# Kernel optimization log

Measured on AMD Instinct MI355X. Metric: run time of the kernel, lower is better.

The kernel has to match this reference:

```python
import jax, jax.numpy as jnp
from jax import lax
import numpy as np

B, N, C, NPOINT, K = 8, 4096, 64, 1024, 32
EPS = 1e-5
SLOPE = 0.1  # leakyrelu negative_slope


def setup_inputs() -> dict:
    key = jax.random.key(0)
    ks = jax.random.split(key, 8)
    d = {
        "xyz": jax.random.normal(ks[0], (B, N, 3), jnp.float32),
        "features": jax.random.normal(ks[1], (B, N, C), jnp.float32),
    }
    for i, n in enumerate(["w_t", "w1_0", "w2_0", "w1_1", "w2_1"]):
        d[n] = jax.random.normal(ks[2 + i], (C, C), jnp.float32) * 0.05
    for n in ["b_t", "b1_0", "b2_0", "b1_1", "b2_1"]:
        d[n] = jnp.zeros((C,), jnp.float32)
    for n in ["g_t", "g1_0", "g2_0", "g1_1", "g2_1"]:
        d[n] = jnp.ones((C,), jnp.float32)
    for n in ["beta_t", "beta1_0", "beta2_0", "beta1_1", "beta2_1"]:
        d[n] = jnp.zeros((C,), jnp.float32)
    return d


def leaky(x):
    return jnp.where(x >= 0, x, SLOPE * x)


def conv1(x, w, b):  # x: [M, Cin, K], w: [Cout, Cin] (1x1 conv)
    return jnp.einsum('mck,oc->mok', x, w) + b[None, :, None]


def bn(x, g, be):  # training-mode BatchNorm1d over (batch, spatial)
    mean = x.mean(axis=(0, 2), keepdims=True)
    var = x.var(axis=(0, 2), keepdims=True)
    return g[None, :, None] * (x - mean) / jnp.sqrt(var + EPS) + be[None, :, None]


def fps(xyz, npoint):
    """Farthest point sampling, deterministic start at index 0. -> [B, npoint] int32"""
    b, n, _ = xyz.shape
    def step(carry, _):
        dist, far = carry
        centroid = jnp.take_along_axis(xyz, far[:, None, None], axis=1)  # [B,1,3]
        d = jnp.sum((xyz - centroid) ** 2, -1)  # [B,N]
        dist = jnp.minimum(dist, d)
        return (dist, jnp.argmax(dist, -1)), far
    init = (jnp.full((b, n), 1e10, xyz.dtype), jnp.zeros((b,), jnp.int32))
    _, idxs = lax.scan(step, init, None, length=npoint)  # [npoint, B]
    return idxs.T


def sqdist(src, dst):  # [B,S,3],[B,N,3] -> [B,S,N]
    d = -2.0 * jnp.einsum('bsc,bnc->bsn', src, dst)
    d += jnp.sum(src ** 2, -1)[:, :, None]
    d += jnp.sum(dst ** 2, -1)[:, None, :]
    return d


def resblock(x, w1, b1, g1, be1, w2, b2, g2, be2):
    h = leaky(bn(conv1(x, w1, b1), g1, be1))
    h = bn(conv1(h, w2, b2), g2, be2)
    return leaky(h + x)


def reference(xyz, features, w_t, b_t, g_t, beta_t,
              w1_0, b1_0, g1_0, beta1_0, w2_0, b2_0, g2_0, beta2_0,
              w1_1, b1_1, g1_1, beta1_1, w2_1, b2_1, g2_1, beta2_1):
    fps_idx = fps(xyz, NPOINT)                                   # [B,S]
    new_xyz = jnp.take_along_axis(xyz, fps_idx[:, :, None], axis=1)  # [B,S,3]
    d = sqdist(new_xyz, xyz)                                     # [B,S,N]
    _, idx = lax.top_k(-d, K)                                    # k smallest -> [B,S,K]
    grouped = jax.vmap(lambda f, i: f[i])(features, idx)         # [B,S,K,C]
    x = grouped.transpose(0, 1, 3, 2).reshape(B * NPOINT, C, K)  # [B*S, C, K]
    x = leaky(bn(conv1(x, w_t, b_t), g_t, beta_t))
    x = resblock(x, w1_0, b1_0, g1_0, beta1_0, w2_0, b2_0, g2_0, beta2_0)
    x = resblock(x, w1_1, b1_1, g1_1, beta1_1, w2_1, b2_1, g2_1, beta2_1)
    nf = x.reshape(B, NPOINT, C, K).transpose(0, 2, 1, 3)        # [B,C,S,K]
    sub_features = nf.max(axis=-1)                               # [B,C,S]
    return (new_xyz.transpose(0, 2, 1), sub_features)
```

## Files before the change

### kernel.cpp

```cpp
#include <hip/hip_runtime.h>
#include <stdint.h>

#define NB 8
#define NN 4096
#define NC 64
#define NS 1024
#define NK 32
#define NQ (NB*NS)
#define NP (NQ*NK)
#define EPSBN 1e-5f

typedef unsigned long long u64;
typedef unsigned short u16;
typedef float v2f __attribute__((ext_vector_type(2)));
typedef short bf8_t __attribute__((ext_vector_type(8)));
typedef float f4_t __attribute__((ext_vector_type(4)));

__device__ __forceinline__ float lrelu(float x){ return x >= 0.0f ? x : 0.1f*x; }

__device__ __forceinline__ unsigned int fkey(float d){
    unsigned int fb = __float_as_uint(d);
    return (fb & 0x80000000u) ? ~fb : (fb | 0x80000000u);
}
__device__ __forceinline__ unsigned f2bf(float f){
    unsigned u = __float_as_uint(f);
    return (u + 0x7fffu + ((u >> 16) & 1u)) >> 16;
}
__device__ __forceinline__ float bflo(unsigned u){ return __uint_as_float(u << 16); }
__device__ __forceinline__ float bfhi(unsigned u){ return __uint_as_float(u & 0xffff0000u); }

__device__ __forceinline__ int wave_incl_add(int x){
    int v = x;
    {int o=__builtin_amdgcn_update_dpp(0,v,0x111,0xf,0xf,true); v+=o;}
    {int o=__builtin_amdgcn_update_dpp(0,v,0x112,0xf,0xf,true); v+=o;}
    {int o=__builtin_amdgcn_update_dpp(0,v,0x114,0xf,0xf,true); v+=o;}
    {int o=__builtin_amdgcn_update_dpp(0,v,0x118,0xf,0xf,true); v+=o;}
    {int o=__builtin_amdgcn_update_dpp(0,v,0x142,0xa,0xf,true); v+=o;}
    {int o=__builtin_amdgcn_update_dpp(0,v,0x143,0xc,0xf,true); v+=o;}
    return v;
}
__device__ __forceinline__ float row_sum16(float x){
    int v = __float_as_int(x);
    {int o=__builtin_amdgcn_update_dpp(0,v,0x111,0xf,0xf,true); v=__float_as_int(__int_as_float(v)+__int_as_float(o));}
    {int o=__builtin_amdgcn_update_dpp(0,v,0x112,0xf,0xf,true); v=__float_as_int(__int_as_float(v)+__int_as_float(o));}
    {int o=__builtin_amdgcn_update_dpp(0,v,0x114,0xf,0xf,true); v=__float_as_int(__int_as_float(v)+__int_as_float(o));}
    {int o=__builtin_amdgcn_update_dpp(0,v,0x118,0xf,0xf,true); v=__float_as_int(__int_as_float(v)+__int_as_float(o));}
    return __int_as_float(v);
}
__device__ __forceinline__ double wave_max_d(double x){
    int lo = __double2loint(x), hi = __double2hiint(x);
    #define FPS_STG(ctl) { \
        int nl=__builtin_amdgcn_update_dpp(lo,lo,ctl,0xf,0xf,false); \
        int nh=__builtin_amdgcn_update_dpp(hi,hi,ctl,0xf,0xf,false); \
        double mx=fmax(__hiloint2double(hi,lo), __hiloint2double(nh,nl)); \
        lo=__double2loint(mx); hi=__double2hiint(mx); }
    FPS_STG(0x111) FPS_STG(0x112) FPS_STG(0x114) FPS_STG(0x118) FPS_STG(0x142) FPS_STG(0x143)
    #undef FPS_STG
    int flo = __builtin_amdgcn_readlane(lo, 63);
    int fhi = __builtin_amdgcn_readlane(hi, 63);
    return __hiloint2double(fhi, flo);
}

__global__ __launch_bounds__(256,1) void fps_kernel(const float* __restrict__ xyz,
                                                    float* __restrict__ out0,
                                                    float* __restrict__ nxyz)
{
    __shared__ float4 sP[NN];
    __shared__ double slots[2][4];
    __shared__ int sFar[NS];
    const int b = blockIdx.x, t = threadIdx.x;
    const int lane = t & 63, wv = t >> 6;
    const float* base = xyz + (size_t)b*NN*3;
    for (int i = t; i < NN; i += 256){
        const float* pp = base + 3*i;
        sP[i] = (float4){pp[0], pp[1], pp[2], 0.0f};
    }
    __syncthreads();
    v2f PX[8], PY[8], PZ[8], D[8];
    int LO[16];
    const int pb = t*16;
    #pragma unroll
    for (int j = 0; j < 8; ++j){
        float4 p0 = sP[pb+2*j], p1 = sP[pb+2*j+1];
        PX[j] = (v2f){ p0.x, p1.x };
        PY[j] = (v2f){ p0.y, p1.y };
        PZ[j] = (v2f){ p0.z, p1.z };
        D[j]  = (v2f){ 1e10f, 1e10f };
    }
    #pragma unroll
    for (int j = 0; j < 16; ++j) LO[j] = (int)(~(unsigned)(pb + j));
    int far = 0;
    float cx = sP[0].x, cy = sP[0].y, cz = sP[0].z;
    for (int s = 0; s < NS; ++s){
        if (t == 255) sFar[s] = far;
        double best;
        {
            #pragma clang fp contract(off)
            v2f cx2 = (v2f){cx, cx}, cy2 = (v2f){cy, cy}, cz2 = (v2f){cz, cz};
            double b0 = -1.0, b1 = -1.0, b2 = -1.0, b3 = -1.0;
            #pragma unroll
            for (int j = 0; j < 8; ++j){
                v2f dx = PX[j] - cx2;
                v2f dy = PY[j] - cy2;
                v2f dz = PZ[j] - cz2;
                v2f dd = (dx*dx + dy*dy) + dz*dz;
                v2f nd = __builtin_elementwise_min(D[j], dd);
                D[j] = nd;
                double k0 = __hiloint2double(__float_as_int(nd.x), LO[2*j]);
                double k1 = __hiloint2double(__float_as_int(nd.y), LO[2*j+1]);
                if (j & 1){ b1 = fmax(b1, k0); b3 = fmax(b3, k1); }
                else      { b0 = fmax(b0, k0); b2 = fmax(b2, k1); }
            }
            best = fmax(fmax(b0, b1), fmax(b2, b3));
        }
        double wb = wave_max_d(best);
        const int par = s & 1;
        if (lane == 0) slots[par][wv] = wb;
        __syncthreads();
        double s0 = slots[par][0], s1 = slots[par][1];
        double s2 = slots[par][2], s3 = slots[par][3];
        double mm = fmax(fmax(s0, s1), fmax(s2, s3));
        far = (int)(~(unsigned)__double2loint(mm));
        float4 cc = sP[far];
        cx = cc.x; cy = cc.y; cz = cc.z;
    }
    __syncthreads();
    for (int s = t; s < NS; s += 256){
        const int f = sFar[s];
        float4 cc = sP[f];
        float* npq = nxyz + ((size_t)b*NS + s)*3;
        npq[0]=cc.x; npq[1]=cc.y; npq[2]=cc.z;
        out0[(b*3+0)*NS+s]=cc.x; out0[(b*3+1)*NS+s]=cc.y; out0[(b*3+2)*NS+s]=cc.z;
    }
}

__global__ __launch_bounds__(256,2) void knn_kernel(const float* __restrict__ xyz,
                                                    const float* __restrict__ nxyz,
                                                    int* __restrict__ kidx)
{
    const int t = threadIdx.x, lane = t & 63, w = t >> 6;
    const int q = blockIdx.x*4 + w;
    const int b = q >> 10;
    const float* base = xyz + (size_t)b*NN*3;
    const float* qp = nxyz + (size_t)q*3;
    const float qx = qp[0], qy = qp[1], qz = qp[2];
    const float qsq = __fadd_rn(__fadd_rn(__fmul_rn(qx,qx),__fmul_rn(qy,qy)),__fmul_rn(qz,qz));

    unsigned int key[64];
    #pragma unroll
    for (int i = 0; i < 64; ++i){
        const int idx = (i<<6) + lane;
        const float* pp = base + 3*idx;
        float x = pp[0], y = pp[1], z = pp[2];
        float dot = __fadd_rn(__fadd_rn(__fmul_rn(qx,x),__fmul_rn(qy,y)),__fmul_rn(qz,z));
        float psq = __fadd_rn(__fadd_rn(__fmul_rn(x,x),__fmul_rn(y,y)),__fmul_rn(z,z));
        float d = __fadd_rn(__fadd_rn(__fmul_rn(-2.0f,dot),qsq),psq);
        key[i] = fkey(d);
    }
    unsigned int pref = 0; int need = 32;
    for (int bit = 31; bit >= 0; --bit){
        const unsigned int bound = 1u << bit;
        int c = 0;
        #pragma unroll
        for (int i = 0; i < 64; ++i) c += ((key[i] ^ pref) < bound) ? 1 : 0;
        int tot = __builtin_amdgcn_readlane(wave_incl_add(c), 63);
        if (tot < need){ need -= tot; pref |= bound; }
    }
    const unsigned int T = pref;
    int cl = 0;
    #pragma unroll
    for (int i = 0; i < 64; ++i) cl += (key[i] < T) ? 1 : 0;
    int incl_cl = wave_incl_add(cl);
    int clx = incl_cl - cl;
    int tiebase = __builtin_amdgcn_readlane(incl_cl, 63);
    int* oq = kidx + (size_t)q*NK;
    int pos = clx;
    #pragma unroll
    for (int i = 0; i < 64; ++i){
        if (key[i] < T){ oq[pos] = (i<<6) + lane; ++pos; }
    }
    int tcount = 0;
    for (int i = 0; i < 64 && tcount < need; ++i){
        u64 m = __ballot(key[i] == T);
        int myrank = (int)__popcll(m & ((1ull << lane) - 1ull));
        if ((key[i] == T) && (tcount + myrank < need))
            oq[tiebase + tcount + myrank] = (i<<6) + lane;
        tcount += (int)__popcll(m);
    }
}

__global__ __launch_bounds__(256) void wtrans_kernel(const float* __restrict__ w0,
    const float* __restrict__ w1, const float* __restrict__ w2,
    const float* __restrict__ w3, const float* __restrict__ w4,
    u16* __restrict__ dst, float* __restrict__ sums)
{
    const float* s;
    switch (blockIdx.x){
        case 0: s = w0; break; case 1: s = w1; break; case 2: s = w2; break;
        case 3: s = w3; break; default: s = w4; break;
    }
    for (int i = threadIdx.x; i < 128; i += 256)
        sums[(size_t)blockIdx.x*128 + i] = 0.0f;
    u16* d = dst + (size_t)blockIdx.x*4096;
    for (int i = threadIdx.x; i < 4096; i += 256){
        const int f = i >> 9, lane = (i >> 3) & 63, j = i & 7;
        const int mt = f >> 1, h = f & 1;
        const int o = mt*16 + (lane & 15);
        const int c = h*32 + (lane >> 4)*8 + j;
        d[i] = (u16)f2bf(s[o*64 + c]);
    }
}

__device__ __forceinline__ void bn_affine_prologue(const float* __restrict__ sums,
    const float* __restrict__ g, const float* __restrict__ beta, float* sAff, int t)
{
    if (t < 64){
        float su = sums[t], sq = sums[64+t];
        float mean = su * (1.0f/(float)NP);
        float var  = fmaxf(sq * (1.0f/(float)NP) - mean*mean, 0.0f);
        float sc = g[t] * rsqrtf(var + EPSBN);
        sAff[t]    = sc;
        sAff[64+t] = beta[t] - mean*sc;
    }
}

template<int ACT>
__global__ __launch_bounds__(256,3) void conv_mfma_kernel(const u16* __restrict__ in,
    u16* __restrict__ out, const u16* __restrict__ wfrag, const float* __restrict__ bias,
    const float* __restrict__ sums, const float* __restrict__ g,
    const float* __restrict__ beta, float* __restrict__ pout)
{
    __shared__ float sStat[4*128];
    __shared__ float sAff[128];
    const int t = threadIdx.x, lane = t & 63, wv = t >> 6;
    const int n = lane & 15, q = lane >> 4;
    const int bb = blockIdx.x;

    float scr[16], shr[16];
    if (ACT){
        bn_affine_prologue(sums, g, beta, sAff, t);
        __syncthreads();
        #pragma unroll
        for (int h = 0; h < 2; ++h){
            float4 a0 = *(const float4*)(sAff + h*32 + q*8);
            float4 a1 = *(const float4*)(sAff + h*32 + q*8 + 4);
            float4 b0 = *(const float4*)(sAff + 64 + h*32 + q*8);
            float4 b1 = *(const float4*)(sAff + 64 + h*32 + q*8 + 4);
            scr[h*8+0]=a0.x; scr[h*8+1]=a0.y; scr[h*8+2]=a0.z; scr[h*8+3]=a0.w;
            scr[h*8+4]=a1.x; scr[h*8+5]=a1.y; scr[h*8+6]=a1.z; scr[h*8+7]=a1.w;
            shr[h*8+0]=b0.x; shr[h*8+1]=b0.y; shr[h*8+2]=b0.z; shr[h*8+3]=b0.w;
            shr[h*8+4]=b1.x; shr[h*8+5]=b1.y; shr[h*8+6]=b1.z; shr[h*8+7]=b1.w;
        }
    }
    bf8_t wf[8];
    #pragma unroll
    for (int f = 0; f < 8; ++f)
        wf[f] = *(const bf8_t*)(wfrag + (f*64 + lane)*8);
    f4_t bv[4];
    #pragma unroll
    for (int mt = 0; mt < 4; ++mt)
        bv[mt] = *(const f4_t*)(bias + mt*16 + q*4);

    float st1[16], st2[16];
    #pragma unroll
    for (int e = 0; e < 16; ++e){ st1[e] = 0.0f; st2[e] = 0.0f; }

    #pragma unroll
    for (int i = 0; i < 4; ++i){
        const int p0 = bb*256 + wv*64 + i*16;
        const u16* row = in + (size_t)(p0 + n)*64;
        bf8_t bf0, bf1;
        if (ACT){
            union { unsigned u[4]; bf8_t v; } B0, B1;
            uint4 r0 = *(const uint4*)(row + q*8);
            uint4 r1 = *(const uint4*)(row + 32 + q*8);
            const unsigned ra[4] = {r0.x, r0.y, r0.z, r0.w};
            const unsigned rb[4] = {r1.x, r1.y, r1.z, r1.w};
            #pragma unroll
            for (int d = 0; d < 4; ++d){
                float x0 = bflo(ra[d]), x1 = bfhi(ra[d]);
                float y0 = fmaf(scr[2*d],   x0, shr[2*d]);   y0 = lrelu(y0);
                float y1 = fmaf(scr[2*d+1], x1, shr[2*d+1]); y1 = lrelu(y1);
                B0.u[d] = f2bf(y0) | (f2bf(y1) << 16);
                float z0 = bflo(rb[d]), z1 = bfhi(rb[d]);
                float w0 = fmaf(scr[8+2*d],   z0, shr[8+2*d]);   w0 = lrelu(w0);
                float w1 = fmaf(scr[8+2*d+1], z1, shr[8+2*d+1]); w1 = lrelu(w1);
                B1.u[d] = f2bf(w0) | (f2bf(w1) << 16);
            }
            bf0 = B0.v; bf1 = B1.v;
        } else {
            bf0 = *(const bf8_t*)(row + q*8);
            bf1 = *(const bf8_t*)(row + 32 + q*8);
        }
        f4_t acc[4];
        #pragma unroll
        for (int mt = 0; mt < 4; ++mt){
            acc[mt] = (f4_t){0.f,0.f,0.f,0.f};
            acc[mt] = __builtin_amdgcn_mfma_f32_16x16x32_bf16(wf[mt*2+0], bf0, acc[mt], 0,0,0);
            acc[mt] = __builtin_amdgcn_mfma_f32_16x16x32_bf16(wf[mt*2+1], bf1, acc[mt], 0,0,0);
        }
        u16* orow = out + (size_t)(p0 + n)*64;
        #pragma unroll
        for (int mt = 0; mt < 4; ++mt){
            float v0 = acc[mt].x + bv[mt].x;
            float v1 = acc[mt].y + bv[mt].y;
            float v2 = acc[mt].z + bv[mt].z;
            float v3 = acc[mt].w + bv[mt].w;
            st1[mt*4+0] += v0; st2[mt*4+0] += v0*v0;
            st1[mt*4+1] += v1; st2[mt*4+1] += v1*v1;
            st1[mt*4+2] += v2; st2[mt*4+2] += v2*v2;
            st1[mt*4+3] += v3; st2[mt*4+3] += v3*v3;
            uint2 pk;
            pk.x = f2bf(v0) | (f2bf(v1) << 16);
            pk.y = f2bf(v2) | (f2bf(v3) << 16);
            *(uint2*)(orow + mt*16 + q*4) = pk;
        }
    }
    #pragma unroll
    for (int e = 0; e < 16; ++e){
        float r1 = row_sum16(st1[e]);
        float r2 = row_sum16(st2[e]);
        if (n == 15){
            const int ch = (e >> 2)*16 + q*4 + (e & 3);
            sStat[wv*128 + ch]      = r1;
            sStat[wv*128 + 64 + ch] = r2;
        }
    }
    __syncthreads();
    if (t < 128){
        float s = sStat[t] + sStat[128+t] + sStat[256+t] + sStat[384+t];
        atomicAdd(pout + t, s);
    }
}

__global__ __launch_bounds__(256,3) void gconv_mfma_kernel(const float* __restrict__ features,
    const int* __restrict__ kidx, u16* __restrict__ out,
    const u16* __restrict__ wfrag, const float* __restrict__ bias,
    float* __restrict__ pout)
{
    __shared__ float sStat[4*128];
    const int t = threadIdx.x, lane = t & 63, wv = t >> 6;
    const int n = lane & 15, q = lane >> 4;
    const int bb = blockIdx.x;

    bf8_t wf[8];
    #pragma unroll
    for (int f = 0; f < 8; ++f)
        wf[f] = *(const bf8_t*)(wfrag + (f*64 + lane)*8);
    f4_t bv[4];
    #pragma unroll
    for (int mt = 0; mt < 4; ++mt)
        bv[mt] = *(const f4_t*)(bias + mt*16 + q*4);

    float st1[16], st2[16];
    #pragma unroll
    for (int e = 0; e < 16; ++e){ st1[e] = 0.0f; st2[e] = 0.0f; }

    #pragma unroll
    for (int i = 0; i < 4; ++i){
        const int p0 = bb*256 + wv*64 + i*16;
        const int p = p0 + n;
        const int b = p >> 15;
        const int idx = kidx[p];
        const float* frow = features + ((size_t)b*NN + idx)*NC;
        union { unsigned u[4]; bf8_t v; } B0, B1;
        {
            float4 a0 = *(const float4*)(frow + q*8);
            float4 a1 = *(const float4*)(frow + q*8 + 4);
            B0.u[0] = f2bf(a0.x) | (f2bf(a0.y) << 16);
            B0.u[1] = f2bf(a0.z) | (f2bf(a0.w) << 16);
            B0.u[2] = f2bf(a1.x) | (f2bf(a1.y) << 16);
            B0.u[3] = f2bf(a1.z) | (f2bf(a1.w) << 16);
            float4 c0 = *(const float4*)(frow + 32 + q*8);
            float4 c1 = *(const float4*)(frow + 32 + q*8 + 4);
            B1.u[0] = f2bf(c0.x) | (f2bf(c0.y) << 16);
            B1.u[1] = f2bf(c0.z) | (f2bf(c0.w) << 16);
            B1.u[2] = f2bf(c1.x) | (f2bf(c1.y) << 16);
            B1.u[3] = f2bf(c1.z) | (f2bf(c1.w) << 16);
        }
        f4_t acc[4];
        #pragma unroll
        for (int mt = 0; mt < 4; ++mt){
            acc[mt] = (f4_t){0.f,0.f,0.f,0.f};
            acc[mt] = __builtin_amdgcn_mfma_f32_16x16x32_bf16(wf[mt*2+0], B0.v, acc[mt], 0,0,0);
            acc[mt] = __builtin_amdgcn_mfma_f32_16x16x32_bf16(wf[mt*2+1], B1.v, acc[mt], 0,0,0);
        }
        u16* orow = out + (size_t)p*64;
        #pragma unroll
        for (int mt = 0; mt < 4; ++mt){
            float v0 = acc[mt].x + bv[mt].x;
            float v1 = acc[mt].y + bv[mt].y;
            float v2 = acc[mt].z + bv[mt].z;
            float v3 = acc[mt].w + bv[mt].w;
            st1[mt*4+0] += v0; st2[mt*4+0] += v0*v0;
            st1[mt*4+1] += v1; st2[mt*4+1] += v1*v1;
            st1[mt*4+2] += v2; st2[mt*4+2] += v2*v2;
            st1[mt*4+3] += v3; st2[mt*4+3] += v3*v3;
            uint2 pk;
            pk.x = f2bf(v0) | (f2bf(v1) << 16);
            pk.y = f2bf(v2) | (f2bf(v3) << 16);
            *(uint2*)(orow + mt*16 + q*4) = pk;
        }
    }
    #pragma unroll
    for (int e = 0; e < 16; ++e){
        float r1 = row_sum16(st1[e]);
        float r2 = row_sum16(st2[e]);
        if (n == 15){
            const int ch = (e >> 2)*16 + q*4 + (e & 3);
            sStat[wv*128 + ch]      = r1;
            sStat[wv*128 + 64 + ch] = r2;
        }
    }
    __syncthreads();
    if (t < 128){
        float s = sStat[t] + sStat[128+t] + sStat[256+t] + sStat[384+t];
        atomicAdd(pout + t, s);
    }
}

__global__ __launch_bounds__(256,2) void resid_kernel(const u16* __restrict__ v,
    const u16* __restrict__ yt, u16* __restrict__ x2,
    const float* __restrict__ sumsV, const float* __restrict__ gV, const float* __restrict__ betaV,
    const float* __restrict__ sumsY, const float* __restrict__ gY, const float* __restrict__ betaY)
{
    __shared__ float sAV[128], sAY[128];
    const int t = threadIdx.x;
    bn_affine_prologue(sumsV, gV, betaV, sAV, t);
    if (t >= 64 && t < 128) bn_affine_prologue(sumsY, gY, betaY, sAY, t - 64);
    __syncthreads();
    const int dc = t & 31, rg = t >> 5;
    const int c0 = dc*2, c1 = c0 + 1;
    const float va0 = sAV[c0], vb0 = sAV[64+c0];
    const float va1 = sAV[c1], vb1 = sAV[64+c1];
    const float ya0 = sAY[c0], yb0 = sAY[64+c0];
    const float ya1 = sAY[c1], yb1 = sAY[64+c1];
    const unsigned* vp = (const unsigned*)v;
    const unsigned* yp = (const unsigned*)yt;
    unsigned* xp = (unsigned*)x2;
    const size_t base = (size_t)blockIdx.x*512;
    #pragma unroll 4
    for (int r = rg; r < 512; r += 8){
        const size_t e = (base + r)*32 + dc;
        unsigned uv = vp[e], uy = yp[e];
        float r0 = lrelu(fmaf(va0, bflo(uv), vb0) + lrelu(fmaf(ya0, bflo(uy), yb0)));
        float r1 = lrelu(fmaf(va1, bfhi(uv), vb1) + lrelu(fmaf(ya1, bfhi(uy), yb1)));
        xp[e] = f2bf(r0) | (f2bf(r1) << 16);
    }
}

__global__ __launch_bounds__(256,2) void final_kernel(const u16* __restrict__ v2,
    const u16* __restrict__ x2,
    const float* __restrict__ sums, const float* __restrict__ g, const float* __restrict__ beta,
    float* __restrict__ out1)
{
    __shared__ float sAff[128];
    const int t = threadIdx.x;
    bn_affine_prologue(sums, g, beta, sAff, t);
    __syncthreads();
    const int dc = t & 31, sg = t >> 5;
    const int c0 = dc*2, c1 = c0 + 1;
    const float a0 = sAff[c0], s0 = sAff[64+c0];
    const float a1 = sAff[c1], s1 = sAff[64+c1];
    const int s = blockIdx.x*8 + sg;
    const unsigned* vp = (const unsigned*)v2;
    const unsigned* xp = (const unsigned*)x2;
    float m0 = -3.0e38f, m1 = -3.0e38f;
    #pragma unroll 8
    for (int kk = 0; kk < 32; ++kk){
        const size_t e = ((size_t)s*32 + kk)*32 + dc;
        unsigned uv = vp[e], ux = xp[e];
        m0 = fmaxf(m0, lrelu(fmaf(a0, bflo(uv), s0) + bflo(ux)));
        m1 = fmaxf(m1, lrelu(fmaf(a1, bfhi(uv), s1) + bfhi(ux)));
    }
    const int b = s >> 10, sl = s & 1023;
    out1[((size_t)b*NC + c0)*NS + sl] = m0;
    out1[((size_t)b*NC + c1)*NS + sl] = m1;
}

extern "C" void kernel_launch(void* const* d_in, const int* in_sizes, int n_in,
                              void* d_out, int out_size, void* d_ws, size_t ws_size,
                              hipStream_t stream)
{
    const float* xyz      = (const float*)d_in[0];
    const float* features = (const float*)d_in[1];
    const float* w_t    = (const float*)d_in[2];
    const float* w1_0   = (const float*)d_in[3];
    const float* w2_0   = (const float*)d_in[4];
    const float* w1_1   = (const float*)d_in[5];
    const float* w2_1   = (const float*)d_in[6];
    const float* b_t    = (const float*)d_in[7];
    const float* b1_0   = (const float*)d_in[8];
    const float* b2_0   = (const float*)d_in[9];
    const float* b1_1   = (const float*)d_in[10];
    const float* b2_1   = (const float*)d_in[11];
    const float* g_t    = (const float*)d_in[12];
    const float* g1_0   = (const float*)d_in[13];
    const float* g2_0   = (const float*)d_in[14];
    const float* g1_1   = (const float*)d_in[15];
    const float* g2_1   = (const float*)d_in[16];
    const float* beta_t  = (const float*)d_in[17];
    const float* beta1_0 = (const float*)d_in[18];
    const float* beta2_0 = (const float*)d_in[19];
    const float* beta1_1 = (const float*)d_in[20];
    const float* beta2_1 = (const float*)d_in[21];

    float* out = (float*)d_out;

    float* nxyz = (float*)d_ws;
    int*   kidx = (int*)(nxyz + 24576);
    float* sums = (float*)(kidx + NP);
    u16*  bwt  = (u16*)(sums + 5*128);
    u16*  buf0 = bwt + 5*4096;
    u16*  buf1 = buf0 + (size_t)NP*NC;
    u16*  buf2 = buf1 + (size_t)NP*NC;

    float* sumsT  = sums + 0*128;
    float* sums10 = sums + 1*128;
    float* sums20 = sums + 2*128;
    float* sums11 = sums + 3*128;
    float* sums21 = sums + 4*128;

    wtrans_kernel<<<5, 256, 0, stream>>>(w_t, w1_0, w2_0, w1_1, w2_1, bwt, sums);
    fps_kernel<<<NB, 256, 0, stream>>>(xyz, out, nxyz);
    knn_kernel<<<NQ/4, 256, 0, stream>>>(xyz, nxyz, kidx);

    gconv_mfma_kernel<<<1024, 256, 0, stream>>>(features, kidx, buf1,
                                                bwt + 0*4096, b_t, sumsT);
    conv_mfma_kernel<1><<<1024, 256, 0, stream>>>(buf1, buf0, bwt + 1*4096, b1_0,
                                                  sumsT, g_t, beta_t, sums10);
    conv_mfma_kernel<1><<<1024, 256, 0, stream>>>(buf0, buf2, bwt + 2*4096, b2_0,
                                                  sums10, g1_0, beta1_0, sums20);
    resid_kernel<<<512, 256, 0, stream>>>(buf2, buf1, buf0,
                                          sums20, g2_0, beta2_0,
                                          sumsT, g_t, beta_t);
    conv_mfma_kernel<0><<<1024, 256, 0, stream>>>(buf0, buf1, bwt + 3*4096, b1_1,
                                                  nullptr, nullptr, nullptr, sums11);
    conv_mfma_kernel<1><<<1024, 256, 0, stream>>>(buf1, buf2, bwt + 4*4096, b2_1,
                                                  sums11, g1_1, beta1_1, sums21);
    final_kernel<<<1024, 256, 0, stream>>>(buf2, buf0,
                                           sums21, g2_1, beta2_1,
                                           out + (size_t)NB*3*NS);
}
```

Measured before the change: 1.010 ms.

## Overlap features bf16 conversion with FPS, spread BN stat atomics, SoA FPS points

Adds 512 extra blocks to the FPS launch that convert features to bf16 into a scratch buffer while the 8 FPS blocks run, so gconv reads pre-converted bf16 rows instead of converting floats per gather. BN statistic atomics are spread over 16 replica slots per channel to reduce atomic contention, and the prologue sums the replicas. FPS shared memory is switched from float4 AoS to separate X/Y/Z arrays, and its max reduction is collapsed into a single serial chain. Risks include FPS-block scheduling interference from the extra blocks and a longer dependency chain in the FPS inner loop.

```diff
diff --git a/kernel.cpp b/kernel.cpp
--- a/kernel.cpp
+++ b/kernel.cpp
@@ -9,6 +9,7 @@
 #define NQ (NB*NS)
 #define NP (NQ*NK)
 #define EPSBN 1e-5f
+#define NREP 16
 
 typedef unsigned long long u64;
 typedef unsigned short u16;
@@ -63,9 +64,24 @@
 
 __global__ __launch_bounds__(256,1) void fps_kernel(const float* __restrict__ xyz,
                                                     float* __restrict__ out0,
-                                                    float* __restrict__ nxyz)
-{
-    __shared__ float4 sP[NN];
+                                                    float* __restrict__ nxyz,
+                                                    const float* __restrict__ features,
+                                                    u16* __restrict__ fbf)
+{
+    if (blockIdx.x >= NB){
+        const int cb = blockIdx.x - NB;
+        const float4* src = (const float4*)features;
+        uint2* dst = (uint2*)fbf;
+        for (int i = cb*256 + threadIdx.x; i < NB*NN*NC/4; i += 512*256){
+            float4 v = src[i];
+            uint2 pk;
+            pk.x = f2bf(v.x) | (f2bf(v.y) << 16);
+            pk.y = f2bf(v.z) | (f2bf(v.w) << 16);
+            dst[i] = pk;
+        }
+        return;
+    }
+    __shared__ float sX[NN], sY[NN], sZ[NN];
     __shared__ double slots[2][4];
     __shared__ int sFar[NS];
     const int b = blockIdx.x, t = threadIdx.x;
@@ -73,7 +89,7 @@
     const float* base = xyz + (size_t)b*NN*3;
     for (int i = t; i < NN; i += 256){
         const float* pp = base + 3*i;
-        sP[i] = (float4){pp[0], pp[1], pp[2], 0.0f};
+        sX[i] = pp[0]; sY[i] = pp[1]; sZ[i] = pp[2];
     }
     __syncthreads();
     v2f PX[8], PY[8], PZ[8], D[8];
@@ -81,23 +97,22 @@
     const int pb = t*16;
     #pragma unroll
     for (int j = 0; j < 8; ++j){
-        float4 p0 = sP[pb+2*j], p1 = sP[pb+2*j+1];
-        PX[j] = (v2f){ p0.x, p1.x };
-        PY[j] = (v2f){ p0.y, p1.y };
-        PZ[j] = (v2f){ p0.z, p1.z };
+        PX[j] = (v2f){ sX[pb+2*j], sX[pb+2*j+1] };
+        PY[j] = (v2f){ sY[pb+2*j], sY[pb+2*j+1] };
+        PZ[j] = (v2f){ sZ[pb+2*j], sZ[pb+2*j+1] };
         D[j]  = (v2f){ 1e10f, 1e10f };
     }
     #pragma unroll
     for (int j = 0; j < 16; ++j) LO[j] = (int)(~(unsigned)(pb + j));
     int far = 0;
-    float cx = sP[0].x, cy = sP[0].y, cz = sP[0].z;
+    float cx = sX[0], cy = sY[0], cz = sZ[0];
     for (int s = 0; s < NS; ++s){
         if (t == 255) sFar[s] = far;
         double best;
         {
             #pragma clang fp contract(off)
             v2f cx2 = (v2f){cx, cx}, cy2 = (v2f){cy, cy}, cz2 = (v2f){cz, cz};
-            double b0 = -1.0, b1 = -1.0, b2 = -1.0, b3 = -1.0;
+            best = -1.0;
             #pragma unroll
             for (int j = 0; j < 8; ++j){
                 v2f dx = PX[j] - cx2;
@@ -106,12 +121,9 @@
                 v2f dd = (dx*dx + dy*dy) + dz*dz;
                 v2f nd = __builtin_elementwise_min(D[j], dd);
                 D[j] = nd;
-                double k0 = __hiloint2double(__float_as_int(nd.x), LO[2*j]);
-                double k1 = __hiloint2double(__float_as_int(nd.y), LO[2*j+1]);
-                if (j & 1){ b1 = fmax(b1, k0); b3 = fmax(b3, k1); }
-                else      { b0 = fmax(b0, k0); b2 = fmax(b2, k1); }
+                best = fmax(best, __hiloint2double(__float_as_int(nd.x), LO[2*j]));
+                best = fmax(best, __hiloint2double(__float_as_int(nd.y), LO[2*j+1]));
             }
-            best = fmax(fmax(b0, b1), fmax(b2, b3));
         }
         double wb = wave_max_d(best);
         const int par = s & 1;
@@ -121,16 +133,15 @@
         double s2 = slots[par][2], s3 = slots[par][3];
         double mm = fmax(fmax(s0, s1), fmax(s2, s3));
         far = (int)(~(unsigned)__double2loint(mm));
-        float4 cc = sP[far];
-        cx = cc.x; cy = cc.y; cz = cc.z;
+        cx = sX[far]; cy = sY[far]; cz = sZ[far];
     }
     __syncthreads();
     for (int s = t; s < NS; s += 256){
         const int f = sFar[s];
-        float4 cc = sP[f];
+        const float x = sX[f], y = sY[f], z = sZ[f];
         float* npq = nxyz + ((size_t)b*NS + s)*3;
-        npq[0]=cc.x; npq[1]=cc.y; npq[2]=cc.z;
-        out0[(b*3+0)*NS+s]=cc.x; out0[(b*3+1)*NS+s]=cc.y; out0[(b*3+2)*NS+s]=cc.z;
+        npq[0]=x; npq[1]=y; npq[2]=z;
+        out0[(b*3+0)*NS+s]=x; out0[(b*3+1)*NS+s]=y; out0[(b*3+2)*NS+s]=z;
     }
 }
 
@@ -199,8 +210,8 @@
         case 0: s = w0; break; case 1: s = w1; break; case 2: s = w2; break;
         case 3: s = w3; break; default: s = w4; break;
     }
-    for (int i = threadIdx.x; i < 128; i += 256)
-        sums[(size_t)blockIdx.x*128 + i] = 0.0f;
+    for (int i = threadIdx.x; i < 128*NREP; i += 256)
+        sums[(size_t)blockIdx.x*128*NREP + i] = 0.0f;
     u16* d = dst + (size_t)blockIdx.x*4096;
     for (int i = threadIdx.x; i < 4096; i += 256){
         const int f = i >> 9, lane = (i >> 3) & 63, j = i & 7;
@@ -215,7 +226,14 @@
     const float* __restrict__ g, const float* __restrict__ beta, float* sAff, int t)
 {
     if (t < 64){
-        float su = sums[t], sq = sums[64+t];
+        const float4* a = (const float4*)(sums + (size_t)t*NREP);
+        const float4* c = (const float4*)(sums + (size_t)(64+t)*NREP);
+        float4 a0=a[0], a1=a[1], a2=a[2], a3=a[3];
+        float4 c0=c[0], c1=c[1], c2=c[2], c3=c[3];
+        float su = ((a0.x+a0.y)+(a0.z+a0.w)) + ((a1.x+a1.y)+(a1.z+a1.w))
+                 + ((a2.x+a2.y)+(a2.z+a2.w)) + ((a3.x+a3.y)+(a3.z+a3.w));
+        float sq = ((c0.x+c0.y)+(c0.z+c0.w)) + ((c1.x+c1.y)+(c1.z+c1.w))
+                 + ((c2.x+c2.y)+(c2.z+c2.w)) + ((c3.x+c3.y)+(c3.z+c3.w));
         float mean = su * (1.0f/(float)NP);
         float var  = fmaxf(sq * (1.0f/(float)NP) - mean*mean, 0.0f);
         float sc = g[t] * rsqrtf(var + EPSBN);
@@ -329,11 +347,11 @@
     __syncthreads();
     if (t < 128){
         float s = sStat[t] + sStat[128+t] + sStat[256+t] + sStat[384+t];
-        atomicAdd(pout + t, s);
-    }
-}
-
-__global__ __launch_bounds__(256,3) void gconv_mfma_kernel(const float* __restrict__ features,
+        atomicAdd(pout + (size_t)t*NREP + (bb & (NREP-1)), s);
+    }
+}
+
+__global__ __launch_bounds__(256,3) void gconv_mfma_kernel(const u16* __restrict__ fbf,
     const int* __restrict__ kidx, u16* __restrict__ out,
     const u16* __restrict__ wfrag, const float* __restrict__ bias,
     float* __restrict__ pout)
@@ -362,28 +380,15 @@
         const int p = p0 + n;
         const int b = p >> 15;
         const int idx = kidx[p];
-        const float* frow = features + ((size_t)b*NN + idx)*NC;
-        union { unsigned u[4]; bf8_t v; } B0, B1;
-        {
-            float4 a0 = *(const float4*)(frow + q*8);
-            float4 a1 = *(const float4*)(frow + q*8 + 4);
-            B0.u[0] = f2bf(a0.x) | (f2bf(a0.y) << 16);
-            B0.u[1] = f2bf(a0.z) | (f2bf(a0.w) << 16);
-            B0.u[2] = f2bf(a1.x) | (f2bf(a1.y) << 16);
-            B0.u[3] = f2bf(a1.z) | (f2bf(a1.w) << 16);
-            float4 c0 = *(const float4*)(frow + 32 + q*8);
-            float4 c1 = *(const float4*)(frow + 32 + q*8 + 4);
-            B1.u[0] = f2bf(c0.x) | (f2bf(c0.y) << 16);
-            B1.u[1] = f2bf(c0.z) | (f2bf(c0.w) << 16);
-            B1.u[2] = f2bf(c1.x) | (f2bf(c1.y) << 16);
-            B1.u[3] = f2bf(c1.z) | (f2bf(c1.w) << 16);
-        }
+        const u16* frow = fbf + ((size_t)b*NN + idx)*NC;
+        bf8_t bf0 = *(const bf8_t*)(frow + q*8);
+        bf8_t bf1 = *(const bf8_t*)(frow + 32 + q*8);
         f4_t acc[4];
         #pragma unroll
         for (int mt = 0; mt < 4; ++mt){
             acc[mt] = (f4_t){0.f,0.f,0.f,0.f};
-            acc[mt] = __builtin_amdgcn_mfma_f32_16x16x32_bf16(wf[mt*2+0], B0.v, acc[mt], 0,0,0);
-            acc[mt] = __builtin_amdgcn_mfma_f32_16x16x32_bf16(wf[mt*2+1], B1.v, acc[mt], 0,0,0);
+            acc[mt] = __builtin_amdgcn_mfma_f32_16x16x32_bf16(wf[mt*2+0], bf0, acc[mt], 0,0,0);
+            acc[mt] = __builtin_amdgcn_mfma_f32_16x16x32_bf16(wf[mt*2+1], bf1, acc[mt], 0,0,0);
         }
         u16* orow = out + (size_t)p*64;
         #pragma unroll
@@ -415,7 +420,7 @@
     __syncthreads();
     if (t < 128){
         float s = sStat[t] + sStat[128+t] + sStat[256+t] + sStat[384+t];
-        atomicAdd(pout + t, s);
+        atomicAdd(pout + (size_t)t*NREP + (bb & (NREP-1)), s);
     }
 }
 
@@ -510,22 +515,23 @@
     float* nxyz = (float*)d_ws;
     int*   kidx = (int*)(nxyz + 24576);
     float* sums = (float*)(kidx + NP);
-    u16*  bwt  = (u16*)(sums + 5*128);
+    u16*  bwt  = (u16*)(sums + 5*128*NREP);
     u16*  buf0 = bwt + 5*4096;
     u16*  buf1 = buf0 + (size_t)NP*NC;
     u16*  buf2 = buf1 + (size_t)NP*NC;
-
-    float* sumsT  = sums + 0*128;
-    float* sums10 = sums + 1*128;
-    float* sums20 = sums + 2*128;
-    float* sums11 = sums + 3*128;
-    float* sums21 = sums + 4*128;
+    u16*  fbf  = buf2;
+
+    float* sumsT  = sums + 0*128*NREP;
+    float* sums10 = sums + 1*128*NREP;
+    float* sums20 = sums + 2*128*NREP;
+    float* sums11 = sums + 3*128*NREP;
+    float* sums21 = sums + 4*128*NREP;
 
     wtrans_kernel<<<5, 256, 0, stream>>>(w_t, w1_0, w2_0, w1_1, w2_1, bwt, sums);
-    fps_kernel<<<NB, 256, 0, stream>>>(xyz, out, nxyz);
+    fps_kernel<<<NB + 512, 256, 0, stream>>>(xyz, out, nxyz, features, fbf);
     knn_kernel<<<NQ/4, 256, 0, stream>>>(xyz, nxyz, kidx);
 
-    gconv_mfma_kernel<<<1024, 256, 0, stream>>>(features, kidx, buf1,
+    gconv_mfma_kernel<<<1024, 256, 0, stream>>>(fbf, kidx, buf1,
                                                 bwt + 0*4096, b_t, sumsT);
     conv_mfma_kernel<1><<<1024, 256, 0, stream>>>(buf1, buf0, bwt + 1*4096, b1_0,
                                                   sumsT, g_t, beta_t, sums10);
```

Result: faster. 963.6 us (-4.6%).
